# Optimization experiments

Measured on AMD Instinct MI355X. Metric: run time of the kernel, lower is better.

Reference implementation:

```python
import jax, jax.numpy as jnp
import numpy as np

EPS = 1e-10            # safe_log epsilon
SIGMOID_BETA = 1.0
MLE_STEP_SIZE = 0.01
NUM_MLE_STEPS = 15
ENT_MULT = 0.01        # entropy loss multiplier placeholder
DECAY_MULT = 0.001     # weight decay multiplier placeholder
B, P, N, T = 512, 1024, 1024, 32


def sigmoid(a, beta=SIGMOID_BETA):
    # module's rescaled sigmoid: 2/(1+exp(-beta*a)) - 1, range (-1, 1)
    return 2.0 / (1.0 + jnp.exp(-beta * a)) - 1.0


def tri_basis(a_sig, centers):
    # triangle basis functions: relu(1 - |a - c_j| / width), width = center spacing
    # a_sig [B,N], centers [T] -> [B,N,T]
    width = centers[1] - centers[0]
    return jax.nn.relu(1.0 - jnp.abs(a_sig[..., None] - centers) / width)


def prob_est(a_sig, thetas, centers):
    # per-neuron mixture of triangle kernels; mixture weights = softmax(thetas)
    pi = jax.nn.softmax(thetas, axis=1)               # [N,T]
    return jnp.einsum('bnt,nt->bn', tri_basis(a_sig, centers), pi)  # [B,N]


def log_likelihood(a_sig, thetas, centers):
    return jnp.sum(jnp.log(prob_est(a_sig, thetas, centers) + EPS))


def calc_entropy(probs):
    # per-neuron entropy reduction over the batch axis
    return -jnp.sum(probs * jnp.log(probs + EPS), axis=0)  # [N]


def setup_inputs() -> dict:
    key = jax.random.key(0)
    k0, k1, k2, k3 = jax.random.split(key, 4)
    x = jax.random.normal(k0, (B, P), jnp.float32)
    w_enc = 0.5 * jax.random.normal(k1, (P, N), jnp.float32)   # truncated_normal std 0.5 approx
    b_enc = 0.1 * jax.random.normal(k2, (N,), jnp.float32)
    w_dec = jnp.transpose(w_enc)                                # initialized as w_enc^T
    b_dec = 0.1 * jax.random.normal(k3, (P,), jnp.float32)
    thetas = jnp.ones((N, T), jnp.float32)                      # construct_thetas init
    triangle_centers = jnp.linspace(-1.0, 1.0, T).astype(jnp.float32)  # a_sig range
    return {"x": x, "w_enc": w_enc, "b_enc": b_enc, "w_dec": w_dec,
            "b_dec": b_dec, "thetas": thetas, "triangle_centers": triangle_centers}


def reference(x, w_enc, b_enc, w_dec, b_dec, thetas, triangle_centers):
    # --- inference: relu encoder (noise_var_mult = 0 -> deterministic a) ---
    a = jax.nn.relu(x @ w_enc + b_enc)                # [B,N]
    a_sig = sigmoid(a, SIGMOID_BETA)                  # [B,N] in (-1,1)

    # --- iterative MLE gradient-ascent on thetas (num_mle_steps updates) ---
    ll_grad = jax.grad(lambda th: log_likelihood(a_sig, th, triangle_centers))

    def mle_step(th, _):
        return th + MLE_STEP_SIZE * ll_grad(th), None

    thetas_new, _ = jax.lax.scan(mle_step, thetas, None, length=NUM_MLE_STEPS)

    # --- entropy of the triangle-kernel density estimate ---
    probs = prob_est(a_sig, thetas_new, triangle_centers)   # [B,N]
    a_entropies = calc_entropy(probs)                       # [N]

    # --- decoder / losses ---
    x_hat = a @ w_dec + b_dec                               # [B,P]
    recon_loss = jnp.mean(0.5 * jnp.sum((x - x_hat) ** 2, axis=1))
    entropy_loss = ENT_MULT * jnp.sum(a_entropies)
    # tf.nn.l2_loss(t) = sum(t^2)/2
    decay_loss = 0.5 * DECAY_MULT * (0.5 * jnp.sum(w_enc ** 2) + 0.5 * jnp.sum(w_dec ** 2))
    total_loss = recon_loss + entropy_loss + decay_loss
    return x_hat, a_entropies, total_loss
```

## Files before the change

kernel.cpp:

```cpp
#include <hip/hip_runtime.h>

#define EPSC 1e-10f
#define BDIM 512
#define PDIM 1024
#define NDIM 1024
#define TDIM 32

typedef __attribute__((ext_vector_type(8))) short short8;
typedef __attribute__((ext_vector_type(4))) float f32x4;

static __device__ __forceinline__ short f2bf(float f) {
  unsigned u = __float_as_uint(f);
  unsigned r = (u + 0x7fffu + ((u >> 16) & 1u)) >> 16;
  return (short)r;
}

#define DPP_ADD(v, ctrl) \
  ((v) + __int_as_float(__builtin_amdgcn_update_dpp(0, __float_as_int(v), (ctrl), 0xf, 0xf, true)))

static __device__ __forceinline__ float dpp_sum64(float v) {
  v = DPP_ADD(v, 0x111);
  v = DPP_ADD(v, 0x112);
  v = DPP_ADD(v, 0x114);
  v = DPP_ADD(v, 0x118);
  v = DPP_ADD(v, 0x142);
  v = DPP_ADD(v, 0x143);
  return __int_as_float(__builtin_amdgcn_readlane(__float_as_int(v), 63));
}

static __device__ __forceinline__ float dpp_sum32(float v) {
  v = DPP_ADD(v, 0x111);
  v = DPP_ADD(v, 0x112);
  v = DPP_ADD(v, 0x114);
  v = DPP_ADD(v, 0x118);
  v = DPP_ADD(v, 0x142);
  return __int_as_float(__builtin_amdgcn_readlane(__float_as_int(v), 31));
}

__global__ __launch_bounds__(256) void conv_kernel(
    const float* __restrict__ X, const float* __restrict__ W1, const float* __restrict__ W2,
    short* __restrict__ Xsw, short* __restrict__ T1, short* __restrict__ T2,
    float* __restrict__ pwsq)
{
  int tid = threadIdx.x;
  if (blockIdx.x < 256) {
    int i = blockIdx.x * 256 + tid;
    int m = i >> 7, c = i & 127;
    const float* src = X + (size_t)m * 1024 + c * 8;
    float4 v0 = *(const float4*)src;
    float4 v1 = *(const float4*)(src + 4);
    short8 o;
    o[0] = f2bf(v0.x); o[1] = f2bf(v0.y); o[2] = f2bf(v0.z); o[3] = f2bf(v0.w);
    o[4] = f2bf(v1.x); o[5] = f2bf(v1.y); o[6] = f2bf(v1.z); o[7] = f2bf(v1.w);
    *(short8*)(Xsw + ((size_t)((m >> 4) * 32 + (c >> 2)) * 512) + (c & 3) * 128 + (m & 15) * 8) = o;
    return;
  }
  __shared__ float T[64][65];
  __shared__ float red[4];
  int wb = blockIdx.x - 256;
  int z = wb >> 8;
  int w = wb & 255;
  int r0 = (w >> 4) * 64;
  int c0 = (w & 15) * 64;
  const float* src = z ? W2 : W1;
  short* dst = z ? T2 : T1;
  float wsq = 0.0f;
#pragma unroll
  for (int i = 0; i < 4; ++i) {
    int row = (tid >> 4) + i * 16;
    int col = (tid & 15) << 2;
    float4 v = *(const float4*)(src + (size_t)(r0 + row) * NDIM + c0 + col);
    T[row][col + 0] = v.x; T[row][col + 1] = v.y; T[row][col + 2] = v.z; T[row][col + 3] = v.w;
    wsq = fmaf(v.x, v.x, wsq); wsq = fmaf(v.y, v.y, wsq);
    wsq = fmaf(v.z, v.z, wsq); wsq = fmaf(v.w, v.w, wsq);
  }
  __syncthreads();
  int nl = tid >> 2;
  int kb = (tid & 3) << 4;
  int ng = c0 + nl;
  int nt = ng >> 4, rn = ng & 15;
#pragma unroll
  for (int h = 0; h < 2; ++h) {
    int kg = r0 + kb + 8 * h;
    int kc = kg >> 5, q = (kg >> 3) & 3;
    short8 o;
#pragma unroll
    for (int e = 0; e < 8; ++e) o[e] = f2bf(T[kb + 8 * h + e][nl]);
    *(short8*)(dst + ((size_t)(nt * 32 + kc) * 512) + q * 128 + rn * 8) = o;
  }
#pragma unroll
  for (int d = 32; d >= 1; d >>= 1) wsq += __shfl_xor(wsq, d);
  if ((tid & 63) == 0) red[tid >> 6] = wsq;
  __syncthreads();
  if (tid == 0) pwsq[wb] = red[0] + red[1] + red[2] + red[3];
}

__global__ __launch_bounds__(256) void gemm1_mfma(
    const short* __restrict__ Xsw, const short* __restrict__ Wsw,
    const float* __restrict__ bias, const float* __restrict__ centers,
    short* __restrict__ Absw, float* __restrict__ U, int* __restrict__ ticket)
{
  __shared__ float T2s[32][36];
  int tid = threadIdx.x;
  if (blockIdx.x == 0 && blockIdx.y == 0 && tid == 0) *ticket = 0;
  int lane = tid & 63, wid = tid >> 6;
  int wy = wid >> 1, wx = wid & 1;
  int mt = blockIdx.y * 2 + wy;
  int nt = blockIdx.x * 2 + wx;
  const short* ap = Xsw + (size_t)mt * 16384 + lane * 8;
  const short* bp = Wsw + (size_t)nt * 16384 + lane * 8;
  f32x4 acc = {0.f, 0.f, 0.f, 0.f};
#pragma unroll 8
  for (int kc = 0; kc < 32; ++kc) {
    short8 a = *(const short8*)(ap + kc * 512);
    short8 b = *(const short8*)(bp + kc * 512);
    acc = __builtin_amdgcn_mfma_f32_16x16x32_bf16(a, b, acc, 0, 0, 0);
  }
  int q = lane >> 4, r = lane & 15;
  int nn = nt * 16 + r;
  float bi = bias[nn];
  float c0 = centers[0];
  float invw = 1.0f / (centers[1] - centers[0]);
  short* abase = Absw + ((size_t)(mt * 32 + (nn >> 5)) * 512) + ((nn >> 3) & 3) * 128 + (nn & 7);
#pragma unroll
  for (int rr = 0; rr < 4; ++rr) {
    int rm = q * 4 + rr;
    float a = fmaxf(acc[rr] + bi, 0.0f);
    abase[rm * 8] = f2bf(a);
    T2s[wx * 16 + r][wy * 16 + rm] = (2.0f / (1.0f + __expf(-a)) - 1.0f - c0) * invw;
  }
  __syncthreads();
  int row = tid >> 3;
  int col4 = (tid & 7) << 2;
  float4 uv = make_float4(T2s[row][col4], T2s[row][col4 + 1], T2s[row][col4 + 2], T2s[row][col4 + 3]);
  *(float4*)(U + (size_t)(blockIdx.x * 32 + row) * BDIM + blockIdx.y * 32 + col4) = uv;
}

__global__ __launch_bounds__(256) void gemm2_mfma(
    const short* __restrict__ Absw, const short* __restrict__ Wdsw,
    const float* __restrict__ bias, const float* __restrict__ X,
    float* __restrict__ out, float* __restrict__ precon)
{
  __shared__ float red[4];
  int tid = threadIdx.x;
  int lane = tid & 63, wid = tid >> 6;
  int wy = wid >> 1, wx = wid & 1;
  int mt = blockIdx.y * 2 + wy;
  int nt = blockIdx.x * 2 + wx;
  const short* ap = Absw + (size_t)mt * 16384 + lane * 8;
  const short* bp = Wdsw + (size_t)nt * 16384 + lane * 8;
  f32x4 acc = {0.f, 0.f, 0.f, 0.f};
#pragma unroll 8
  for (int kc = 0; kc < 32; ++kc) {
    short8 a = *(const short8*)(ap + kc * 512);
    short8 b = *(const short8*)(bp + kc * 512);
    acc = __builtin_amdgcn_mfma_f32_16x16x32_bf16(a, b, acc, 0, 0, 0);
  }
  int q = lane >> 4, r = lane & 15;
  int nn = nt * 16 + r;
  float bi = bias[nn];
  float local = 0.0f;
#pragma unroll
  for (int rr = 0; rr < 4; ++rr) {
    int mm = mt * 16 + q * 4 + rr;
    float xh = acc[rr] + bi;
    out[(size_t)mm * PDIM + nn] = xh;
    float d = xh - X[(size_t)mm * PDIM + nn];
    local = fmaf(d, d, local);
  }
#pragma unroll
  for (int d = 32; d >= 1; d >>= 1) local += __shfl_xor(local, d);
  if ((tid & 63) == 0) red[tid >> 6] = local;
  __syncthreads();
  if (tid == 0) precon[blockIdx.y * 32 + blockIdx.x] = red[0] + red[1] + red[2] + red[3];
}

__global__ __launch_bounds__(64) void mle_kernel(
    const float* __restrict__ U, const float* __restrict__ thetas,
    float* __restrict__ ent_out, const float* __restrict__ precon,
    const float* __restrict__ pwsq, int* __restrict__ ticket, float* __restrict__ out)
{
  int n = blockIdx.x;
  int lane = threadIdx.x;
  __shared__ int tick_s;

  const float4* up = (const float4*)(U + (size_t)n * BDIM + lane * 8);
  float4 u0 = up[0], u1 = up[1];
  float uu[8] = {u0.x, u0.y, u0.z, u0.w, u1.x, u1.y, u1.z, u1.w};
  float f[8]; int jl[8];
#pragma unroll
  for (int i = 0; i < 8; ++i) {
    int j = (int)uu[i];
    if (j > 30) j = 30;
    if (j < 15) j = 15;
    f[i] = uu[i] - (float)j;
    jl[i] = j - 15;
  }
  float th = thetas[(size_t)n * TDIM + (lane & 31)];
  int t2 = lane & 31;

#pragma unroll 1
  for (int step = 0; step < 15; ++step) {
    float e = __expf(th);
    float se = dpp_sum32(e);
    float pv = e * __builtin_amdgcn_rcpf(se);

    float pj[8], pj1[8];
#pragma unroll
    for (int i = 0; i < 8; ++i) pj[i] = __shfl(pv, jl[i] + 15);
#pragma unroll
    for (int i = 0; i < 8; ++i) pj1[i] = __shfl(pv, jl[i] + 16);

    float w0[8], w1[8];
#pragma unroll
    for (int i = 0; i < 8; ++i) {
      float p = fmaf(f[i], pj1[i] - pj[i], pj[i]);
      float r = __builtin_amdgcn_rcpf(p + EPSC);
      w0[i] = (1.0f - f[i]) * r;
      w1[i] = f[i] * r;
    }

    float bins[17];
#pragma unroll
    for (int t = 0; t < 17; ++t) bins[t] = 0.0f;
#pragma unroll
    for (int i = 0; i < 8; ++i) {
#pragma unroll
      for (int t = 0; t < 17; ++t)
        bins[t] += (jl[i] == t) ? w0[i] : ((jl[i] == t - 1) ? w1[i] : 0.0f);
    }

    float s[17];
#pragma unroll
    for (int t = 0; t < 17; ++t) s[t] = dpp_sum64(bins[t]);

    float sv = 0.0f;
#pragma unroll
    for (int t = 0; t < 17; ++t) sv = (t2 == t + 15) ? s[t] : sv;
    th += 0.01f * pv * (sv - 512.0f);
  }

  float e = __expf(th);
  float se = dpp_sum32(e);
  float pv = e * __builtin_amdgcn_rcpf(se);
  float pj[8], pj1[8];
#pragma unroll
  for (int i = 0; i < 8; ++i) pj[i] = __shfl(pv, jl[i] + 15);
#pragma unroll
  for (int i = 0; i < 8; ++i) pj1[i] = __shfl(pv, jl[i] + 16);
  float ent = 0.0f;
#pragma unroll
  for (int i = 0; i < 8; ++i) {
    float p = fmaf(f[i], pj1[i] - pj[i], pj[i]);
    ent = fmaf(p, __logf(p + EPSC), ent);
  }
  float etot = dpp_sum64(ent);
  if (lane == 0) ent_out[n] = -etot;

  __threadfence();
  if (lane == 0) tick_s = atomicAdd(ticket, 1);
  __syncthreads();
  if (tick_s == NDIM - 1) {
    __threadfence();
    const volatile float* ev = (const volatile float*)ent_out;
    float acc = 0.0f;
#pragma unroll
    for (int i = 0; i < 16; i++) acc += 0.01f * ev[lane + i * 64];
#pragma unroll
    for (int i = 0; i < 8; i++) acc += (0.5f / (float)BDIM) * precon[lane + i * 64];
#pragma unroll
    for (int i = 0; i < 8; i++) acc += 0.00025f * pwsq[lane + i * 64];
    float tot = dpp_sum64(acc);
    if (lane == 0) out[(size_t)BDIM * PDIM + NDIM] = tot;
  }
}

extern "C" void kernel_launch(void* const* d_in, const int* in_sizes, int n_in,
                              void* d_out, int out_size, void* d_ws, size_t ws_size,
                              hipStream_t stream) {
  (void)in_sizes; (void)n_in; (void)out_size; (void)ws_size;
  const float* x       = (const float*)d_in[0];
  const float* w_enc   = (const float*)d_in[1];
  const float* b_enc   = (const float*)d_in[2];
  const float* w_dec   = (const float*)d_in[3];
  const float* b_dec   = (const float*)d_in[4];
  const float* thetas  = (const float*)d_in[5];
  const float* centers = (const float*)d_in[6];
  float* out = (float*)d_out;

  char* ws = (char*)d_ws;
  short* Xsw    = (short*)(ws);
  short* Wsw    = (short*)(ws + (1 << 20));
  short* Wdsw   = (short*)(ws + (3 << 20));
  short* Absw   = (short*)(ws + (5 << 20));
  float* U      = (float*)(ws + (6 << 20));
  float* precon = (float*)(ws + (8 << 20));
  float* pwsq   = (float*)(ws + (8 << 20) + 4096);
  int*   ticket = (int*)(ws + (8 << 20) + 8192);
  float* ent_out = out + (size_t)BDIM * PDIM;

  hipLaunchKernelGGL(conv_kernel, dim3(768), dim3(256), 0, stream,
                     x, w_enc, w_dec, Xsw, Wsw, Wdsw, pwsq);
  hipLaunchKernelGGL(gemm1_mfma, dim3(32, 16), dim3(256), 0, stream,
                     Xsw, Wsw, b_enc, centers, Absw, U, ticket);
  hipLaunchKernelGGL(gemm2_mfma, dim3(32, 16), dim3(256), 0, stream,
                     Absw, Wdsw, b_dec, x, out, precon);
  hipLaunchKernelGGL(mle_kernel, dim3(NDIM), dim3(64), 0, stream,
                     U, thetas, ent_out, precon, pwsq, ticket, out);
}
```

Measured before the change: 155.2 us.

## Split MLE per-neuron work across four wavefronts with LDS bin reduction

The MLE kernel now uses 256 threads per neuron instead of one 64-lane wavefront, so each lane handles 2 batch samples instead of 8. Per-wave DPP bin sums are combined through a double-buffered shared array with a __syncthreads each step. This cuts serial per-lane work and raises the number of waves in flight. In exchange it adds a block barrier per MLE step and repeats the softmax and bin reductions in every wave.

```diff
diff --git a/kernel.cpp b/kernel.cpp
--- a/kernel.cpp
+++ b/kernel.cpp
@@ -18,14 +18,14 @@
 #define DPP_ADD(v, ctrl) \
   ((v) + __int_as_float(__builtin_amdgcn_update_dpp(0, __float_as_int(v), (ctrl), 0xf, 0xf, true)))
 
-static __device__ __forceinline__ float dpp_sum64(float v) {
+static __device__ __forceinline__ float dpp_sum64_v(float v) {
   v = DPP_ADD(v, 0x111);
   v = DPP_ADD(v, 0x112);
   v = DPP_ADD(v, 0x114);
   v = DPP_ADD(v, 0x118);
   v = DPP_ADD(v, 0x142);
   v = DPP_ADD(v, 0x143);
-  return __int_as_float(__builtin_amdgcn_readlane(__float_as_int(v), 63));
+  return v;
 }
 
 static __device__ __forceinline__ float dpp_sum32(float v) {
@@ -175,29 +175,31 @@
   if (tid == 0) precon[blockIdx.y * 32 + blockIdx.x] = red[0] + red[1] + red[2] + red[3];
 }
 
-__global__ __launch_bounds__(64) void mle_kernel(
+__global__ __launch_bounds__(256) void mle_kernel(
     const float* __restrict__ U, const float* __restrict__ thetas,
     float* __restrict__ ent_out, const float* __restrict__ precon,
     const float* __restrict__ pwsq, int* __restrict__ ticket, float* __restrict__ out)
 {
   int n = blockIdx.x;
-  int lane = threadIdx.x;
+  int tid = threadIdx.x;
+  int lane = tid & 63, w = tid >> 6;
+  int t2 = lane & 31;
+  __shared__ float buf[2][72];
+  __shared__ float entp[4];
   __shared__ int tick_s;
 
-  const float4* up = (const float4*)(U + (size_t)n * BDIM + lane * 8);
-  float4 u0 = up[0], u1 = up[1];
-  float uu[8] = {u0.x, u0.y, u0.z, u0.w, u1.x, u1.y, u1.z, u1.w};
-  float f[8]; int jl[8];
-#pragma unroll
-  for (int i = 0; i < 8; ++i) {
+  float2 uv2 = *(const float2*)(U + (size_t)n * BDIM + w * 128 + lane * 2);
+  float uu[2] = {uv2.x, uv2.y};
+  float f[2]; int jl[2];
+#pragma unroll
+  for (int i = 0; i < 2; ++i) {
     int j = (int)uu[i];
     if (j > 30) j = 30;
     if (j < 15) j = 15;
     f[i] = uu[i] - (float)j;
     jl[i] = j - 15;
   }
-  float th = thetas[(size_t)n * TDIM + (lane & 31)];
-  int t2 = lane & 31;
+  float th = thetas[(size_t)n * TDIM + t2];
 
 #pragma unroll 1
   for (int step = 0; step < 15; ++step) {
@@ -205,15 +207,13 @@
     float se = dpp_sum32(e);
     float pv = e * __builtin_amdgcn_rcpf(se);
 
-    float pj[8], pj1[8];
-#pragma unroll
-    for (int i = 0; i < 8; ++i) pj[i] = __shfl(pv, jl[i] + 15);
-#pragma unroll
-    for (int i = 0; i < 8; ++i) pj1[i] = __shfl(pv, jl[i] + 16);
-
-    float w0[8], w1[8];
-#pragma unroll
-    for (int i = 0; i < 8; ++i) {
+    float pj[2], pj1[2];
+#pragma unroll
+    for (int i = 0; i < 2; ++i) { pj[i] = __shfl(pv, jl[i] + 15); pj1[i] = __shfl(pv, jl[i] + 16); }
+
+    float w0[2], w1[2];
+#pragma unroll
+    for (int i = 0; i < 2; ++i) {
       float p = fmaf(f[i], pj1[i] - pj[i], pj[i]);
       float r = __builtin_amdgcn_rcpf(p + EPSC);
       w0[i] = (1.0f - f[i]) * r;
@@ -224,54 +224,64 @@
 #pragma unroll
     for (int t = 0; t < 17; ++t) bins[t] = 0.0f;
 #pragma unroll
-    for (int i = 0; i < 8; ++i) {
+    for (int i = 0; i < 2; ++i) {
 #pragma unroll
       for (int t = 0; t < 17; ++t)
         bins[t] += (jl[i] == t) ? w0[i] : ((jl[i] == t - 1) ? w1[i] : 0.0f);
     }
 
-    float s[17];
-#pragma unroll
-    for (int t = 0; t < 17; ++t) s[t] = dpp_sum64(bins[t]);
+#pragma unroll
+    for (int t = 0; t < 17; ++t) bins[t] = dpp_sum64_v(bins[t]);
+
+    int par = step & 1;
+    if (lane == 63) {
+#pragma unroll
+      for (int t = 0; t < 17; ++t) buf[par][w * 17 + t] = bins[t];
+    }
+    __syncthreads();
 
     float sv = 0.0f;
-#pragma unroll
-    for (int t = 0; t < 17; ++t) sv = (t2 == t + 15) ? s[t] : sv;
+    if (t2 >= 15) {
+      int b = t2 - 15;
+      sv = buf[par][b] + buf[par][17 + b] + buf[par][34 + b] + buf[par][51 + b];
+    }
     th += 0.01f * pv * (sv - 512.0f);
   }
 
   float e = __expf(th);
   float se = dpp_sum32(e);
   float pv = e * __builtin_amdgcn_rcpf(se);
-  float pj[8], pj1[8];
-#pragma unroll
-  for (int i = 0; i < 8; ++i) pj[i] = __shfl(pv, jl[i] + 15);
-#pragma unroll
-  for (int i = 0; i < 8; ++i) pj1[i] = __shfl(pv, jl[i] + 16);
   float ent = 0.0f;
 #pragma unroll
-  for (int i = 0; i < 8; ++i) {
-    float p = fmaf(f[i], pj1[i] - pj[i], pj[i]);
+  for (int i = 0; i < 2; ++i) {
+    float pj  = __shfl(pv, jl[i] + 15);
+    float pj1 = __shfl(pv, jl[i] + 16);
+    float p = fmaf(f[i], pj1 - pj, pj);
     ent = fmaf(p, __logf(p + EPSC), ent);
   }
-  float etot = dpp_sum64(ent);
-  if (lane == 0) ent_out[n] = -etot;
+  ent = dpp_sum64_v(ent);
+  if (lane == 63) entp[w] = ent;
+  __syncthreads();
+  if (tid == 0) ent_out[n] = -(entp[0] + entp[1] + entp[2] + entp[3]);
 
   __threadfence();
-  if (lane == 0) tick_s = atomicAdd(ticket, 1);
+  if (tid == 0) tick_s = atomicAdd(ticket, 1);
   __syncthreads();
   if (tick_s == NDIM - 1) {
     __threadfence();
     const volatile float* ev = (const volatile float*)ent_out;
     float acc = 0.0f;
 #pragma unroll
-    for (int i = 0; i < 16; i++) acc += 0.01f * ev[lane + i * 64];
-#pragma unroll
-    for (int i = 0; i < 8; i++) acc += (0.5f / (float)BDIM) * precon[lane + i * 64];
-#pragma unroll
-    for (int i = 0; i < 8; i++) acc += 0.00025f * pwsq[lane + i * 64];
-    float tot = dpp_sum64(acc);
-    if (lane == 0) out[(size_t)BDIM * PDIM + NDIM] = tot;
+    for (int i = 0; i < 4; i++) acc += 0.01f * ev[tid + i * 256];
+#pragma unroll
+    for (int i = 0; i < 2; i++) acc += (0.5f / (float)BDIM) * precon[tid + i * 256];
+#pragma unroll
+    for (int i = 0; i < 2; i++) acc += 0.00025f * pwsq[tid + i * 256];
+#pragma unroll
+    for (int d = 32; d >= 1; d >>= 1) acc += __shfl_xor(acc, d);
+    if (lane == 0) entp[w] = acc;
+    __syncthreads();
+    if (tid == 0) out[(size_t)BDIM * PDIM + NDIM] = entp[0] + entp[1] + entp[2] + entp[3];
   }
 }
 
@@ -305,6 +315,6 @@
                      Xsw, Wsw, b_enc, centers, Absw, U, ticket);
   hipLaunchKernelGGL(gemm2_mfma, dim3(32, 16), dim3(256), 0, stream,
                      Absw, Wdsw, b_dec, x, out, precon);
-  hipLaunchKernelGGL(mle_kernel, dim3(NDIM), dim3(64), 0, stream,
+  hipLaunchKernelGGL(mle_kernel, dim3(NDIM), dim3(256), 0, stream,
                      U, thetas, ent_out, precon, pwsq, ticket, out);
 }
```

Result: slower. 182.3 us (+17.5%).
